# Kernel optimization log

Hardware: AMD Instinct MI355X
Metric: run time of the kernel (lower is better)

Reference implementation:

```python
import jax, jax.numpy as jnp
import numpy as np

NUM_CLUSTERS = 32


def setup_inputs() -> dict:
    key = jax.random.key(0)
    k1, k2 = jax.random.split(key)
    B, N, D = 16, 16384, 128
    x = jax.random.normal(k1, (B, N, D), dtype=jnp.float32)
    cluster_ids = jax.random.randint(k2, (B, N), 0, NUM_CLUSTERS, dtype=jnp.int32)
    return {"x": x, "cluster_ids": cluster_ids}


def reference(x, cluster_ids):
    # x: [B, N, D]; cluster_ids: [B, N] int labels in [0, C)
    C = NUM_CLUSTERS
    # One-hot cluster membership: [B, N, C]
    onehot = (cluster_ids[..., None] == jnp.arange(C, dtype=cluster_ids.dtype)).astype(x.dtype)
    counts = onehot.sum(axis=1)                       # [B, C]
    sums = jnp.einsum('bnc,bnd->bcd', onehot, x)      # segment sums [B, C, D]
    # Per-cluster mean; empty clusters -> zero rows (contribute 0 to off-diag Gram)
    means = sums / jnp.maximum(counts, 1.0)[..., None]
    # Pairwise |dot products| between cluster means: [B, C, C]
    gram = jnp.abs(jnp.einsum('bcd,bed->bce', means, means))
    # Strict upper-triangular sum (torch.triu(..., diagonal=1))
    triu_mask = jnp.triu(jnp.ones((C, C), dtype=x.dtype), k=1)
    triu_sum = jnp.sum(gram * triu_mask, axis=(1, 2))  # [B]
    # Number of valid (non-empty) clusters per batch
    valid = jnp.sum(counts > 0, axis=1).astype(x.dtype)
    denom = jnp.where(valid > 1, valid * (valid - 1.0) * 0.5, 1.0)
    return jnp.mean(triu_sum / denom)
```

## Files before the change

### kernel.cpp

```cpp
#include <hip/hip_runtime.h>
#include <hip/hip_bf16.h>

#define BB 16
#define NN 16384
#define DD 128
#define CC 32
#define CHUNKS 32
#define ROWS_PER_BLOCK (NN / CHUNKS)
#define ROWS_PER_WAVE  (ROWS_PER_BLOCK / 4)

__global__ __launch_bounds__(256) void seg_sum_kernel(
    const float* __restrict__ x, const int* __restrict__ ids,
    float* __restrict__ gsums, float* __restrict__ gcounts) {
  __shared__ float lsum[4][CC * DD];
  __shared__ float lcnt[CC];
  __shared__ int   lcid[ROWS_PER_BLOCK];

  const int tid  = threadIdx.x;
  const int b    = blockIdx.y;
  const int row0 = blockIdx.x * ROWS_PER_BLOCK;
  const int lane = tid & 63;
  const int w    = tid >> 6;
  const int* __restrict__ idrow = ids + (size_t)b * NN;

  if (tid < CC) lcnt[tid] = 0.f;
  lcid[tid]       = idrow[row0 + tid];
  lcid[tid + 256] = idrow[row0 + tid + 256];
  {
    const float4 z4 = make_float4(0.f, 0.f, 0.f, 0.f);
#pragma unroll
    for (int i = 0; i < 16; ++i)
      *reinterpret_cast<float4*>(&lsum[w][(i * 64 + lane) * 4]) = z4;
  }
  __syncthreads();
  atomicAdd(&lcnt[lcid[tid]], 1.f);
  atomicAdd(&lcnt[lcid[tid + 256]], 1.f);

  const float2* __restrict__ x2 =
      reinterpret_cast<const float2*>(x + (size_t)b * NN * DD);
  const int wbase = w * ROWS_PER_WAVE;
  float* const slab = &lsum[w][0];

  float2 vA[8], vB[8];
  int cA[8], cB[8];

#define LOADG(V, C, g)                                                     \
  {                                                                        \
    _Pragma("unroll") for (int k = 0; k < 8; ++k) {                        \
      const int rl = wbase + (g) * 8 + k;                                  \
      V[k] = x2[(size_t)(row0 + rl) * 64 + lane];                          \
      C[k] = lcid[rl];                                                     \
    }                                                                      \
  }
#define RMWG(V, C)                                                         \
  {                                                                        \
    _Pragma("unroll") for (int k = 0; k < 8; ++k) {                        \
      float2* p = reinterpret_cast<float2*>(&slab[C[k] * DD + 2 * lane]);  \
      float2 old = *p;                                                     \
      *p = make_float2(old.x + V[k].x, old.y + V[k].y);                    \
    }                                                                      \
  }

  LOADG(vA, cA, 0)
#pragma unroll
  for (int i = 0; i < 7; ++i) {
    LOADG(vB, cB, 2 * i + 1)
    RMWG(vA, cA)
    LOADG(vA, cA, 2 * i + 2)
    RMWG(vB, cB)
  }
  LOADG(vB, cB, 15)
  RMWG(vA, cA)
  RMWG(vB, cB)
#undef LOADG
#undef RMWG
  __syncthreads();

  float* __restrict__ gs = gsums + (size_t)b * CC * DD;
  for (int i = tid; i < CC * DD; i += 256) {
    float s = lsum[0][i] + lsum[1][i] + lsum[2][i] + lsum[3][i];
    atomicAdd(&gs[i], s);
  }
  if (tid < CC) atomicAdd(&gcounts[b * CC + tid], lcnt[tid]);
}

#define MSTR 132
__global__ __launch_bounds__(512) void finish_kernel(
    const float* __restrict__ gsums, const float* __restrict__ gcounts,
    float* __restrict__ out) {
  __shared__ float mean[CC * MSTR];
  __shared__ float cnt[CC];
  __shared__ float red[512];

  const int b = blockIdx.x;
  const int tid = threadIdx.x;

  if (tid < CC) cnt[tid] = gcounts[b * CC + tid];
  __syncthreads();

  for (int i = tid; i < CC * DD; i += 512) {
    int c = i >> 7;
    int d = i & 127;
    mean[c * MSTR + d] = gsums[(size_t)b * CC * DD + i] / fmaxf(cnt[c], 1.f);
  }
  __syncthreads();

  float acc = 0.f;
  if (tid < (CC * (CC - 1)) / 2) {
    int c = 0, rem = tid;
    while (rem >= (CC - 1 - c)) { rem -= (CC - 1 - c); ++c; }
    int e = c + 1 + rem;
    const float4* mc = reinterpret_cast<const float4*>(&mean[c * MSTR]);
    const float4* me = reinterpret_cast<const float4*>(&mean[e * MSTR]);
    float dot = 0.f;
#pragma unroll 8
    for (int j = 0; j < DD / 4; ++j) {
      float4 a = mc[j], bb = me[j];
      dot += a.x * bb.x + a.y * bb.y + a.z * bb.z + a.w * bb.w;
    }
    acc = fabsf(dot);
  }

  red[tid] = acc;
  __syncthreads();
  for (int s = 256; s > 0; s >>= 1) {
    if (tid < s) red[tid] += red[tid + s];
    __syncthreads();
  }

  if (tid == 0) {
    float valid = 0.f;
    for (int c = 0; c < CC; ++c) valid += (cnt[c] > 0.f) ? 1.f : 0.f;
    float denom = (valid > 1.f) ? valid * (valid - 1.f) * 0.5f : 1.f;
    atomicAdd(out, red[0] / denom * (1.0f / BB));
  }
}

extern "C" void kernel_launch(void* const* d_in, const int* in_sizes, int n_in,
                              void* d_out, int out_size, void* d_ws, size_t ws_size,
                              hipStream_t stream) {
  const float* x   = (const float*)d_in[0];
  const int*   ids = (const int*)d_in[1];
  float* out = (float*)d_out;

  float* gsums   = (float*)d_ws;
  float* gcounts = gsums + (size_t)BB * CC * DD;

  const size_t ws_bytes = ((size_t)BB * CC * DD + (size_t)BB * CC) * sizeof(float);
  hipMemsetAsync(d_ws, 0, ws_bytes, stream);
  hipMemsetAsync(d_out, 0, sizeof(float), stream);

  dim3 grid1(CHUNKS, BB);
  seg_sum_kernel<<<grid1, 256, 0, stream>>>(x, ids, gsums, gcounts);
  finish_kernel<<<BB, 512, 0, stream>>>(gsums, gcounts, out);
}
```

Measured before the change: 44.38 us.

## Replace global atomics and memsets with partial buffers and reduction kernels

When the workspace is large enough, each segment-sum block writes its per-cluster partial sums and counts to a private slot with vectorized stores instead of doing global atomicAdds. A new reduction kernel then sums the 32 chunk partials per batch, and a final single-wave kernel adds the per-batch losses. This removes both hipMemsetAsync calls and all atomic contention, at the cost of two extra kernel launches and about 8 MB of partial-buffer traffic. The load/RMW groups are also widened from 8 to 16 rows, which deepens memory-level parallelism but raises register use.

```diff
diff --git a/kernel.cpp b/kernel.cpp
--- a/kernel.cpp
+++ b/kernel.cpp
@@ -6,12 +6,20 @@
 #define DD 128
 #define CC 32
 #define CHUNKS 32
+#define NBLK (BB * CHUNKS)
 #define ROWS_PER_BLOCK (NN / CHUNKS)
 #define ROWS_PER_WAVE  (ROWS_PER_BLOCK / 4)
 
+#define P_SUMS 0
+#define P_CNTS ((size_t)NBLK * CC * DD)
+#define R_SUMS (P_CNTS + (size_t)NBLK * CC)
+#define R_CNTS (R_SUMS + (size_t)BB * CC * DD)
+#define LOSSP  (R_CNTS + (size_t)BB * CC)
+#define WS_A_FLOATS (LOSSP + BB)
+
 __global__ __launch_bounds__(256) void seg_sum_kernel(
     const float* __restrict__ x, const int* __restrict__ ids,
-    float* __restrict__ gsums, float* __restrict__ gcounts) {
+    float* __restrict__ outsums, float* __restrict__ outcnts, int mode) {
   __shared__ float lsum[4][CC * DD];
   __shared__ float lcnt[CC];
   __shared__ int   lcid[ROWS_PER_BLOCK];
@@ -21,6 +29,7 @@
   const int row0 = blockIdx.x * ROWS_PER_BLOCK;
   const int lane = tid & 63;
   const int w    = tid >> 6;
+  const int slot = b * CHUNKS + blockIdx.x;
   const int* __restrict__ idrow = ids + (size_t)b * NN;
 
   if (tid < CC) lcnt[tid] = 0.f;
@@ -41,20 +50,20 @@
   const int wbase = w * ROWS_PER_WAVE;
   float* const slab = &lsum[w][0];
 
-  float2 vA[8], vB[8];
-  int cA[8], cB[8];
+  float2 vA[16], vB[16];
+  int cA[16], cB[16];
 
 #define LOADG(V, C, g)                                                     \
   {                                                                        \
-    _Pragma("unroll") for (int k = 0; k < 8; ++k) {                        \
-      const int rl = wbase + (g) * 8 + k;                                  \
+    _Pragma("unroll") for (int k = 0; k < 16; ++k) {                       \
+      const int rl = wbase + (g) * 16 + k;                                 \
       V[k] = x2[(size_t)(row0 + rl) * 64 + lane];                          \
       C[k] = lcid[rl];                                                     \
     }                                                                      \
   }
 #define RMWG(V, C)                                                         \
   {                                                                        \
-    _Pragma("unroll") for (int k = 0; k < 8; ++k) {                        \
+    _Pragma("unroll") for (int k = 0; k < 16; ++k) {                       \
       float2* p = reinterpret_cast<float2*>(&slab[C[k] * DD + 2 * lane]);  \
       float2 old = *p;                                                     \
       *p = make_float2(old.x + V[k].x, old.y + V[k].y);                    \
@@ -63,31 +72,67 @@
 
   LOADG(vA, cA, 0)
 #pragma unroll
-  for (int i = 0; i < 7; ++i) {
+  for (int i = 0; i < 3; ++i) {
     LOADG(vB, cB, 2 * i + 1)
     RMWG(vA, cA)
     LOADG(vA, cA, 2 * i + 2)
     RMWG(vB, cB)
   }
-  LOADG(vB, cB, 15)
+  LOADG(vB, cB, 7)
   RMWG(vA, cA)
   RMWG(vB, cB)
 #undef LOADG
 #undef RMWG
   __syncthreads();
 
-  float* __restrict__ gs = gsums + (size_t)b * CC * DD;
-  for (int i = tid; i < CC * DD; i += 256) {
-    float s = lsum[0][i] + lsum[1][i] + lsum[2][i] + lsum[3][i];
-    atomicAdd(&gs[i], s);
-  }
-  if (tid < CC) atomicAdd(&gcounts[b * CC + tid], lcnt[tid]);
+  if (mode) {
+    float* __restrict__ ps = outsums + (size_t)slot * CC * DD;
+#pragma unroll
+    for (int it = 0; it < 4; ++it) {
+      const int i = (it * 256 + tid) * 4;
+      float4 s0 = *reinterpret_cast<const float4*>(&lsum[0][i]);
+      float4 s1 = *reinterpret_cast<const float4*>(&lsum[1][i]);
+      float4 s2 = *reinterpret_cast<const float4*>(&lsum[2][i]);
+      float4 s3 = *reinterpret_cast<const float4*>(&lsum[3][i]);
+      float4 r = make_float4(s0.x + s1.x + s2.x + s3.x, s0.y + s1.y + s2.y + s3.y,
+                             s0.z + s1.z + s2.z + s3.z, s0.w + s1.w + s2.w + s3.w);
+      *reinterpret_cast<float4*>(&ps[i]) = r;
+    }
+    if (tid < CC) outcnts[slot * CC + tid] = lcnt[tid];
+  } else {
+    float* __restrict__ gs = outsums + (size_t)b * CC * DD;
+    for (int i = tid; i < CC * DD; i += 256) {
+      float s = lsum[0][i] + lsum[1][i] + lsum[2][i] + lsum[3][i];
+      atomicAdd(&gs[i], s);
+    }
+    if (tid < CC) atomicAdd(&outcnts[b * CC + tid], lcnt[tid]);
+  }
+}
+
+__global__ __launch_bounds__(256) void reduce_partials_kernel(
+    const float* __restrict__ psums, const float* __restrict__ pcnts,
+    float* __restrict__ rsums, float* __restrict__ rcnts) {
+  const int j = blockIdx.x;
+  const int b = j >> 4;
+  const int e0 = (j & 15) * 256;
+  const int tid = threadIdx.x;
+  float s = 0.f;
+#pragma unroll 8
+  for (int c = 0; c < CHUNKS; ++c)
+    s += psums[((size_t)(b * CHUNKS + c)) * CC * DD + e0 + tid];
+  rsums[(size_t)b * CC * DD + e0 + tid] = s;
+  if ((j & 15) == 0 && tid < CC) {
+    float cs = 0.f;
+#pragma unroll 8
+    for (int c = 0; c < CHUNKS; ++c) cs += pcnts[(b * CHUNKS + c) * CC + tid];
+    rcnts[b * CC + tid] = cs;
+  }
 }
 
 #define MSTR 132
 __global__ __launch_bounds__(512) void finish_kernel(
     const float* __restrict__ gsums, const float* __restrict__ gcounts,
-    float* __restrict__ out) {
+    float* __restrict__ lossp, float* __restrict__ out, int mode) {
   __shared__ float mean[CC * MSTR];
   __shared__ float cnt[CC];
   __shared__ float red[512];
@@ -132,8 +177,18 @@
     float valid = 0.f;
     for (int c = 0; c < CC; ++c) valid += (cnt[c] > 0.f) ? 1.f : 0.f;
     float denom = (valid > 1.f) ? valid * (valid - 1.f) * 0.5f : 1.f;
-    atomicAdd(out, red[0] / denom * (1.0f / BB));
-  }
+    float v = red[0] / denom * (1.0f / BB);
+    if (mode) lossp[b] = v;
+    else atomicAdd(out, v);
+  }
+}
+
+__global__ __launch_bounds__(64) void final_kernel(
+    const float* __restrict__ lossp, float* __restrict__ out) {
+  float v = (threadIdx.x < BB) ? lossp[threadIdx.x] : 0.f;
+#pragma unroll
+  for (int o = 8; o > 0; o >>= 1) v += __shfl_down(v, o, 16);
+  if (threadIdx.x == 0) out[0] = v;
 }
 
 extern "C" void kernel_launch(void* const* d_in, const int* in_sizes, int n_in,
@@ -142,15 +197,26 @@
   const float* x   = (const float*)d_in[0];
   const int*   ids = (const int*)d_in[1];
   float* out = (float*)d_out;
-
-  float* gsums   = (float*)d_ws;
-  float* gcounts = gsums + (size_t)BB * CC * DD;
-
-  const size_t ws_bytes = ((size_t)BB * CC * DD + (size_t)BB * CC) * sizeof(float);
-  hipMemsetAsync(d_ws, 0, ws_bytes, stream);
-  hipMemsetAsync(d_out, 0, sizeof(float), stream);
+  float* ws  = (float*)d_ws;
 
   dim3 grid1(CHUNKS, BB);
-  seg_sum_kernel<<<grid1, 256, 0, stream>>>(x, ids, gsums, gcounts);
-  finish_kernel<<<BB, 512, 0, stream>>>(gsums, gcounts, out);
-}
+  if (ws_size >= WS_A_FLOATS * sizeof(float)) {
+    float* psums = ws + P_SUMS;
+    float* pcnts = ws + P_CNTS;
+    float* rsums = ws + R_SUMS;
+    float* rcnts = ws + R_CNTS;
+    float* lossp = ws + LOSSP;
+    seg_sum_kernel<<<grid1, 256, 0, stream>>>(x, ids, psums, pcnts, 1);
+    reduce_partials_kernel<<<256, 256, 0, stream>>>(psums, pcnts, rsums, rcnts);
+    finish_kernel<<<BB, 512, 0, stream>>>(rsums, rcnts, lossp, out, 1);
+    final_kernel<<<1, 64, 0, stream>>>(lossp, out);
+  } else {
+    float* gsums   = ws;
+    float* gcounts = gsums + (size_t)BB * CC * DD;
+    const size_t wsb = ((size_t)BB * CC * DD + (size_t)BB * CC) * sizeof(float);
+    hipMemsetAsync(d_ws, 0, wsb, stream);
+    hipMemsetAsync(d_out, 0, sizeof(float), stream);
+    seg_sum_kernel<<<grid1, 256, 0, stream>>>(x, ids, gsums, gcounts, 0);
+    finish_kernel<<<BB, 512, 0, stream>>>(gsums, gcounts, nullptr, out, 0);
+  }
+}
```

Result: faster. 40.90 us (-7.8%).
